# Optimization experiments

Hardware: AMD Instinct MI355X
Metric: run time of the kernel (lower is better)

The kernel has to match this reference:

```python
import jax, jax.numpy as jnp
import numpy as np

K = 8  # K_num: neighbors per pred point


def setup_inputs() -> dict:
    key = jax.random.key(0)
    ks = jax.random.split(key, 8)
    B, Nr, Np, C = 2, 8192, 8192, 256
    s = 1.0 / np.sqrt(C)
    return {
        "xyz_ref": jax.random.normal(ks[0], (B, Nr, 3), jnp.float32) * 10.0,
        "xyz_pred": jax.random.normal(ks[1], (B, Np, 3), jnp.float32) * 10.0,
        "feat_k_ref": jax.random.normal(ks[2], (B, Nr, C), jnp.float32),
        "feat_q_pred": jax.random.normal(ks[3], (B, Np, C), jnp.float32),
        "feat_v_ref": jax.random.normal(ks[4], (B, Nr, C), jnp.float32),
        "Wv": jax.random.normal(ks[5], (C, C), jnp.float32) * s,
        "bv": jnp.zeros((C,), jnp.float32),
        "Wo": jax.random.normal(ks[6], (C, C), jnp.float32) * s,
        "bo": jnp.zeros((C,), jnp.float32),
        "Wout": jax.random.normal(ks[7], (2 * C, C), jnp.float32) * s,
    }


def reference(xyz_ref, xyz_pred, feat_k_ref, feat_q_pred, feat_v_ref, Wv, bv, Wo, bo, Wout):
    B, Np, C = feat_q_pred.shape
    Nr = feat_k_ref.shape[1]

    # --- KNN search (torch.no_grad in original) ---
    xr = jax.lax.stop_gradient(xyz_ref)
    xp = jax.lax.stop_gradient(xyz_pred)
    d2 = (jnp.sum(xp * xp, -1)[:, :, None]
          + jnp.sum(xr * xr, -1)[:, None, :]
          - 2.0 * jnp.einsum('bpd,brd->bpr', xp, xr))  # [B, Np, Nr]
    _, idx = jax.lax.top_k(-d2, K)  # [B, Np, K] nearest ref indices per pred point

    # --- W_v (Conv1d 1x1) applied to all ref values before gather ---
    v_all = jnp.einsum('brc,dc->brd', feat_v_ref, Wv) + bv  # [B, Nr, C]

    gather = jax.vmap(lambda f, i: f[i])  # per-sample fancy gather
    k = gather(feat_k_ref, idx)  # [B, Np, K, C]
    v = gather(v_all, idx)       # [B, Np, K, C]

    # --- tiny per-point cross attention over K neighbors ---
    scores = jnp.einsum('bpc,bpkc->bpk', feat_q_pred, k) / jnp.sqrt(jnp.asarray(C, feat_q_pred.dtype))
    attn = jax.nn.softmax(scores, axis=-1)          # [B, Np, K]
    out = jnp.einsum('bpk,bpkc->bpc', attn, v)      # [B, Np, C]

    # --- W_o (Conv1d 1x1) ---
    out = jnp.einsum('bpc,dc->bpd', out, Wo) + bo   # [B, Np, C]

    # --- scatter into full point set: ref rows stay zero, pred rows get out ---
    out_all = jnp.concatenate([jnp.zeros((B, Nr, C), out.dtype), out], axis=1)  # [B, Nr+Np, C]

    # --- W_out (MinkowskiConvolution k=1, no bias): C -> 2C ---
    return jnp.einsum('bnc,dc->bnd', out_all, Wout)  # [B, Nr+Np, 2C]
```

## Files before the change

### kernel.cpp

```cpp
#include <hip/hip_runtime.h>
#include <stdint.h>


#define NRr 8192
#define NPp 8192
#define NC  256
#define NK  8
#define NCH   16
#define CHUNK 512

typedef short bf16x8 __attribute__((ext_vector_type(8)));
typedef float f32x4  __attribute__((ext_vector_type(4)));

__device__ __forceinline__ uint16_t f2bf(float f) {
  uint32_t u = __float_as_uint(f);
  return (uint16_t)((u + 0x7fffu + ((u >> 16) & 1u)) >> 16);
}

__device__ __forceinline__ float d2f(float px, float py, float pz, float sp, float4 r) {
  float m0 = __fmul_rn(px, r.x), m1 = __fmul_rn(py, r.y), m2 = __fmul_rn(pz, r.z);
  float dot = __fadd_rn(__fadd_rn(m0, m1), m2);
  return __fsub_rn(__fadd_rn(sp, r.w), __fadd_rn(dot, dot));
}

__device__ __forceinline__ float d2q(float px, float py, float pz, float sp, float4 r) {
  float dot = fmaf(px, r.x, fmaf(py, r.y, pz * r.z));
  return fmaf(-2.f, dot, sp + r.w);
}

#define SLACK 0.0625f

__device__ __forceinline__ uint32_t fkey(float f) {
  uint32_t b = __float_as_uint(f);
  return (b & 0x80000000u) ? ~b : (b | 0x80000000u);
}

__global__ __launch_bounds__(64) void k_prep(const float* __restrict__ xyz_ref,
                                             float4* __restrict__ ref4) {
  int i = blockIdx.x * 64 + threadIdx.x;
  if (i >= 2 * NRr) return;
  float x = xyz_ref[i*3+0];
  float y = xyz_ref[i*3+1];
  float z = xyz_ref[i*3+2];
  float n = __fadd_rn(__fadd_rn(__fmul_rn(x,x), __fmul_rn(y,y)), __fmul_rn(z,z));
  ref4[i] = make_float4(x, y, z, n);
}

__device__ __forceinline__ void insert8(float d2, int j, float (&dist)[8], int (&id)[8]) {
  if (d2 < dist[7]) {
    #pragma unroll
    for (int k = 7; k >= 1; --k) {
      bool sh = d2 < dist[k-1];
      bool pl = d2 < dist[k];
      float nd = sh ? dist[k-1] : (pl ? d2 : dist[k]);
      int   ni = sh ? id[k-1]   : (pl ? j  : id[k]);
      dist[k] = nd; id[k] = ni;
    }
    if (d2 < dist[0]) { dist[0] = d2; id[0] = j; }
  }
}

__global__ __launch_bounds__(256, 5) void k_knn(const float* __restrict__ xyz_pred,
                                                const float4* __restrict__ ref4,
                                                uint16_t* __restrict__ part,
                                                const float* __restrict__ Wv,
                                                const float* __restrict__ bv,
                                                const float* __restrict__ Wo,
                                                const float* __restrict__ bo,
                                                const float* __restrict__ Wout,
                                                uint16_t* __restrict__ Aw,
                                                float* __restrict__ bbig) {
  __shared__ __align__(16) char smem[32768];

  if (blockIdx.x < 64) {
    float (*M8)[256] = (float (*)[256])smem;
    float* red = (float*)(smem + 8192);
    int e0 = blockIdx.x * 8;
    int t  = threadIdx.x;

    float acc8[8];
    #pragma unroll
    for (int e = 0; e < 8; ++e) acc8[e] = 0.f;
    for (int d = 0; d < 256; ++d) {
      float wo = Wo[(size_t)d*256 + t];
      #pragma unroll
      for (int e = 0; e < 8; ++e)
        acc8[e] = fmaf(Wout[(size_t)(e0+e)*256 + d], wo, acc8[e]);
    }
    #pragma unroll
    for (int e = 0; e < 8; ++e) M8[e][t] = acc8[e];
    __syncthreads();

    float a8[8];
    #pragma unroll
    for (int e = 0; e < 8; ++e) a8[e] = 0.f;
    for (int c = 0; c < 256; ++c) {
      float wv = Wv[(size_t)c*256 + t];
      #pragma unroll
      for (int e = 0; e < 8; ++e)
        a8[e] = fmaf(M8[e][c], wv, a8[e]);
    }
    #pragma unroll
    for (int e = 0; e < 8; ++e) Aw[(size_t)(e0+e)*256 + t] = f2bf(a8[e]);

    for (int e = 0; e < 8; ++e) {
      red[t] = fmaf(M8[e][t], bv[t], Wout[(size_t)(e0+e)*256 + t] * bo[t]);
      __syncthreads();
      for (int s2 = 128; s2 > 0; s2 >>= 1) {
        if (t < s2) red[t] += red[t + s2];
        __syncthreads();
      }
      if (t == 0) bbig[e0+e] = red[0];
      __syncthreads();
    }
    return;
  }

  float4* sref = (float4*)smem;
  int wave = threadIdx.x >> 6;
  int lane = threadIdx.x & 63;
  int task = (blockIdx.x - 64) * 4 + wave;
  int ch   = task & (NCH - 1);
  int P    = (task >> 4) * 64 + lane;
  int b    = P >> 13;

  float px = xyz_pred[P*3+0];
  float py = xyz_pred[P*3+1];
  float pz = xyz_pred[P*3+2];
  float sp = __fadd_rn(__fadd_rn(__fmul_rn(px,px), __fmul_rn(py,py)), __fmul_rn(pz,pz));

  const float4* refbase = ref4 + (size_t)b * NRr;
  int rbase = ch * CHUNK;
  float4* srefw = sref + wave * CHUNK;
  for (int j = lane; j < CHUNK; j += 64) srefw[j] = refbase[rbase + j];

  float a0 = 3.4e38f, a1 = 3.4e38f, a2 = 3.4e38f, a3 = 3.4e38f;
  float g0 = 3.4e38f, g1 = 3.4e38f, g2 = 3.4e38f, g3 = 3.4e38f;
  float dist[8]; int id[8];
  #pragma unroll
  for (int k = 0; k < 8; ++k) { dist[k] = 3.4e38f; id[k] = 0; }

  for (int s = 0; s < CHUNK / 32; ++s) {
    uint32_t mm = 0;
    int base = s * 32;
    #pragma unroll 4
    for (int jj = 0; jj < 32; jj += 2) {
      float d0 = d2q(px, py, pz, sp, srefw[base + jj]);
      float d1 = d2q(px, py, pz, sp, srefw[base + jj + 1]);
      a3 = __builtin_amdgcn_fmed3f(d0, a2, a3);
      a2 = __builtin_amdgcn_fmed3f(d0, a1, a2);
      a1 = __builtin_amdgcn_fmed3f(d0, a0, a1);
      a0 = fminf(d0, a0);
      g3 = __builtin_amdgcn_fmed3f(d1, g2, g3);
      g2 = __builtin_amdgcn_fmed3f(d1, g1, g2);
      g1 = __builtin_amdgcn_fmed3f(d1, g0, g1);
      g0 = fminf(d1, g0);
      float tau = fmaxf(a3, g3) + SLACK;
      mm |= (uint32_t)(d0 <= tau) << jj;
      mm |= (uint32_t)(d1 <= tau) << (jj + 1);
    }
    while (mm) {
      int bit = __builtin_ctz(mm); mm &= mm - 1;
      int j = base + bit;
      float dd = d2f(px, py, pz, sp, srefw[j]);
      insert8(dd, j, dist, id);
    }
  }

  uint16_t* pp = part + ((size_t)P * NCH + ch) * 8;
  #pragma unroll
  for (int k = 0; k < 8; ++k)
    pp[k] = (uint16_t)((rbase + id[k]) & (NRr - 1));
}

__global__ __launch_bounds__(256) void k_attn(const float* __restrict__ feat_q,
    const float* __restrict__ feat_k, const float* __restrict__ feat_v,
    const uint16_t* __restrict__ part, const float* __restrict__ xyz_pred,
    const float4* __restrict__ ref4, uint16_t* __restrict__ g) {
  int wave = threadIdx.x >> 6;
  int lane = threadIdx.x & 63;
  int P = blockIdx.x * 4 + wave;
  int b = P >> 13;

  float px = xyz_pred[P*3+0];
  float py = xyz_pred[P*3+1];
  float pz = xyz_pred[P*3+2];
  float sp = __fadd_rn(__fadd_rn(__fmul_rn(px,px), __fmul_rn(py,py)), __fmul_rn(pz,pz));
  const float4* refbase = ref4 + (size_t)b * NRr;

  const uint32_t* pw = (const uint32_t*)(part + (size_t)P * (NCH * 8));
  uint32_t two = pw[lane];
  int j0 = two & (NRr - 1);
  int j1 = (two >> 16) & (NRr - 1);
  float d0 = d2f(px, py, pz, sp, refbase[j0]);
  float d1 = d2f(px, py, pz, sp, refbase[j1]);
  uint64_t k0 = ((uint64_t)fkey(d0) << 32) | (uint32_t)j0;
  uint64_t k1 = ((uint64_t)fkey(d1) << 32) | (uint32_t)j1;

  int nb[8];
  #pragma unroll
  for (int r = 0; r < 8; ++r) {
    uint64_t m = (k0 < k1) ? k0 : k1;
    #pragma unroll
    for (int s = 1; s < 64; s <<= 1) {
      uint64_t o = __shfl_xor(m, s, 64);
      m = (o < m) ? o : m;
    }
    nb[r] = (int)(uint32_t)(m & 0xFFFFFFFFu) & (NRr - 1);
    if (k0 == m) k0 = ~0ULL;
    if (k1 == m) k1 = ~0ULL;
  }

  float4 qv = *(const float4*)(feat_q + (size_t)P*NC + lane*4);
  const float* kb = feat_k + (size_t)b * NRr * NC;
  const float* vb = feat_v + (size_t)b * NRr * NC;

  float s[8];
  #pragma unroll
  for (int k = 0; k < 8; ++k) {
    float4 kv = *(const float4*)(kb + (size_t)nb[k]*NC + lane*4);
    float p = qv.x * kv.x;
    p = fmaf(qv.y, kv.y, p);
    p = fmaf(qv.z, kv.z, p);
    p = fmaf(qv.w, kv.w, p);
    s[k] = p;
  }
  #pragma unroll
  for (int k = 0; k < 8; ++k) {
    float v = s[k];
    #pragma unroll
    for (int m = 1; m < 64; m <<= 1) v += __shfl_xor(v, m, 64);
    s[k] = v * 0.0625f;
  }
  float mx = s[0];
  #pragma unroll
  for (int k = 1; k < 8; ++k) mx = fmaxf(mx, s[k]);
  float e[8], sum = 0.f;
  #pragma unroll
  for (int k = 0; k < 8; ++k) { e[k] = expf(s[k] - mx); sum += e[k]; }
  float inv = 1.0f / sum;

  float g0 = 0.f, g1 = 0.f, g2 = 0.f, g3 = 0.f;
  #pragma unroll
  for (int k = 0; k < 8; ++k) {
    float4 vv = *(const float4*)(vb + (size_t)nb[k]*NC + lane*4);
    float w = e[k] * inv;
    g0 = fmaf(w, vv.x, g0);
    g1 = fmaf(w, vv.y, g1);
    g2 = fmaf(w, vv.z, g2);
    g3 = fmaf(w, vv.w, g3);
  }
  uint32_t p0 = ((uint32_t)f2bf(g1) << 16) | f2bf(g0);
  uint32_t p1 = ((uint32_t)f2bf(g3) << 16) | f2bf(g2);
  *(uint2*)(g + (size_t)P*NC + lane*4) = make_uint2(p0, p1);
}

__global__ void k_zero(float4* __restrict__ o) {
  int i = blockIdx.x * 256 + threadIdx.x;
  int b = i >> 20;
  int r = i & 1048575;
  o[(size_t)b * 2097152 + r] = make_float4(0.f, 0.f, 0.f, 0.f);
}

__global__ __launch_bounds__(256) void k_gemm(const uint16_t* __restrict__ g,
    const uint16_t* __restrict__ Aw, const float* __restrict__ bbig,
    float* __restrict__ outp) {
  __shared__ __align__(16) uint16_t sA[64 * 136];
  __shared__ __align__(16) uint16_t sB[64 * 136];
  int t = threadIdx.x;
  int lane = t & 63, wave = t >> 6;
  int wm = (wave >> 1) * 32, wn = (wave & 1) * 32;
  int q = lane >> 4, rr = lane & 15;
  int bm = blockIdx.x;
  int bn = blockIdx.y;
  f32x4 zero = {0.f, 0.f, 0.f, 0.f};
  f32x4 acc[2][2] = {{zero, zero}, {zero, zero}};

  for (int ph = 0; ph < 2; ++ph) {
    #pragma unroll
    for (int i = 0; i < 4; ++i) {
      int cc  = t + i * 256;
      int row = cc >> 4;
      int col = (cc & 15) << 3;
      uint4 da = *(const uint4*)(g  + ((size_t)(bm*64 + row))*NC + ph*128 + col);
      *(uint4*)(&sA[row*136 + col]) = da;
      uint4 db = *(const uint4*)(Aw + ((size_t)(bn*64 + row))*NC + ph*128 + col);
      *(uint4*)(&sB[row*136 + col]) = db;
    }
    __syncthreads();
    #pragma unroll
    for (int kk = 0; kk < 4; ++kk) {
      int ko = kk*32 + q*8;
      bf16x8 a0 = *(const bf16x8*)(&sA[(wm      + rr)*136 + ko]);
      bf16x8 a1 = *(const bf16x8*)(&sA[(wm + 16 + rr)*136 + ko]);
      bf16x8 b0 = *(const bf16x8*)(&sB[(wn      + rr)*136 + ko]);
      bf16x8 b1 = *(const bf16x8*)(&sB[(wn + 16 + rr)*136 + ko]);
      acc[0][0] = __builtin_amdgcn_mfma_f32_16x16x32_bf16(a0, b0, acc[0][0], 0, 0, 0);
      acc[0][1] = __builtin_amdgcn_mfma_f32_16x16x32_bf16(a0, b1, acc[0][1], 0, 0, 0);
      acc[1][0] = __builtin_amdgcn_mfma_f32_16x16x32_bf16(a1, b0, acc[1][0], 0, 0, 0);
      acc[1][1] = __builtin_amdgcn_mfma_f32_16x16x32_bf16(a1, b1, acc[1][1], 0, 0, 0);
    }
    __syncthreads();
  }
  #pragma unroll
  for (int j = 0; j < 2; ++j) {
    int col = bn*64 + wn + j*16 + rr;
    float bias = bbig[col];
    #pragma unroll
    for (int i = 0; i < 2; ++i) {
      #pragma unroll
      for (int r = 0; r < 4; ++r) {
        int row = bm*64 + wm + i*16 + q*4 + r;
        float v = acc[i][j][r] + bias;
        int bb = row >> 13, p = row & 8191;
        outp[((size_t)(bb*16384 + 8192 + p))*512 + col] = v;
      }
    }
  }
}

extern "C" void kernel_launch(void* const* d_in, const int* in_sizes, int n_in,
                              void* d_out, int out_size, void* d_ws, size_t ws_size,
                              hipStream_t stream) {
  const float* xyz_ref  = (const float*)d_in[0];
  const float* xyz_pred = (const float*)d_in[1];
  const float* feat_k   = (const float*)d_in[2];
  const float* feat_q   = (const float*)d_in[3];
  const float* feat_v   = (const float*)d_in[4];
  const float* Wv       = (const float*)d_in[5];
  const float* bv       = (const float*)d_in[6];
  const float* Wo       = (const float*)d_in[7];
  const float* bo       = (const float*)d_in[8];
  const float* Wout     = (const float*)d_in[9];
  float* outp = (float*)d_out;

  char* ob = (char*)d_out;
  uint16_t* g    = (uint16_t*)ob;
  float4*   ref4 = (float4*)(ob + 8388608);
  uint16_t* Aw   = (uint16_t*)(ob + 9175040);
  float*    bbig = (float*)(ob + 9437184);
  uint16_t* part = (uint16_t*)(ob + 33554432);

  k_prep   <<<256,  64,  0, stream>>>(xyz_ref, ref4);
  k_knn    <<<1088, 256, 0, stream>>>(xyz_pred, ref4, part,
                                      Wv, bv, Wo, bo, Wout, Aw, bbig);
  k_attn   <<<4096, 256, 0, stream>>>(feat_q, feat_k, feat_v, part,
                                      xyz_pred, ref4, g);
  k_gemm   <<<dim3(256, 8), 256, 0, stream>>>(g, Aw, bbig, outp);
  k_zero   <<<8192, 256, 0, stream>>>((float4*)outp);
}
```

Baseline: 283.8 us.

## Assign one wave per pred point in KNN and merge top-8 inside the kernel

The KNN kernel used to give each lane its own pred point and split the ref set into 16 chunks, writing partial top-8 lists that k_attn then re-scored and merged. Now each wave handles a single pred point: lanes stride over shared-memory tiles of refs, each lane keeps a local top-8, and a wave-wide shuffle reduction produces the final 8 indices, which go straight to an idx buffer. k_attn reads only those indices, which removes the partial-list traffic and the recompute-and-merge step. The cost is more blocks with block-level syncs per tile and a per-point shuffle merge inside KNN.

```diff
diff --git a/kernel.cpp b/kernel.cpp
--- a/kernel.cpp
+++ b/kernel.cpp
@@ -6,8 +6,8 @@
 #define NPp 8192
 #define NC  256
 #define NK  8
-#define NCH   16
-#define CHUNK 512
+#define TILE 1024
+#define NT   8
 
 typedef short bf16x8 __attribute__((ext_vector_type(8)));
 typedef float f32x4  __attribute__((ext_vector_type(4)));
@@ -60,9 +60,9 @@
   }
 }
 
-__global__ __launch_bounds__(256, 5) void k_knn(const float* __restrict__ xyz_pred,
+__global__ __launch_bounds__(256, 8) void k_knn(const float* __restrict__ xyz_pred,
                                                 const float4* __restrict__ ref4,
-                                                uint16_t* __restrict__ part,
+                                                int* __restrict__ idx,
                                                 const float* __restrict__ Wv,
                                                 const float* __restrict__ bv,
                                                 const float* __restrict__ Wo,
@@ -70,7 +70,7 @@
                                                 const float* __restrict__ Wout,
                                                 uint16_t* __restrict__ Aw,
                                                 float* __restrict__ bbig) {
-  __shared__ __align__(16) char smem[32768];
+  __shared__ __align__(16) char smem[16384];
 
   if (blockIdx.x < 64) {
     float (*M8)[256] = (float (*)[256])smem;
@@ -116,12 +116,11 @@
     return;
   }
 
-  float4* sref = (float4*)smem;
+  float4* tile = (float4*)smem;
+  int kb   = blockIdx.x - 64;
   int wave = threadIdx.x >> 6;
   int lane = threadIdx.x & 63;
-  int task = (blockIdx.x - 64) * 4 + wave;
-  int ch   = task & (NCH - 1);
-  int P    = (task >> 4) * 64 + lane;
+  int P    = kb * 4 + wave;
   int b    = P >> 13;
 
   float px = xyz_pred[P*3+0];
@@ -130,9 +129,6 @@
   float sp = __fadd_rn(__fadd_rn(__fmul_rn(px,px), __fmul_rn(py,py)), __fmul_rn(pz,pz));
 
   const float4* refbase = ref4 + (size_t)b * NRr;
-  int rbase = ch * CHUNK;
-  float4* srefw = sref + wave * CHUNK;
-  for (int j = lane; j < CHUNK; j += 64) srefw[j] = refbase[rbase + j];
 
   float a0 = 3.4e38f, a1 = 3.4e38f, a2 = 3.4e38f, a3 = 3.4e38f;
   float g0 = 3.4e38f, g1 = 3.4e38f, g2 = 3.4e38f, g3 = 3.4e38f;
@@ -140,13 +136,20 @@
   #pragma unroll
   for (int k = 0; k < 8; ++k) { dist[k] = 3.4e38f; id[k] = 0; }
 
-  for (int s = 0; s < CHUNK / 32; ++s) {
+  for (int t = 0; t < NT; ++t) {
+    int tb = t * TILE;
+    #pragma unroll
+    for (int u = 0; u < 4; ++u)
+      tile[threadIdx.x + u*256] = refbase[tb + threadIdx.x + u*256];
+    __syncthreads();
+
     uint32_t mm = 0;
-    int base = s * 32;
     #pragma unroll 4
-    for (int jj = 0; jj < 32; jj += 2) {
-      float d0 = d2q(px, py, pz, sp, srefw[base + jj]);
-      float d1 = d2q(px, py, pz, sp, srefw[base + jj + 1]);
+    for (int i = 0; i < 16; i += 2) {
+      float4 r0 = tile[i*64 + lane];
+      float4 r1 = tile[(i+1)*64 + lane];
+      float d0 = d2q(px, py, pz, sp, r0);
+      float d1 = d2q(px, py, pz, sp, r1);
       a3 = __builtin_amdgcn_fmed3f(d0, a2, a3);
       a2 = __builtin_amdgcn_fmed3f(d0, a1, a2);
       a1 = __builtin_amdgcn_fmed3f(d0, a0, a1);
@@ -156,60 +159,52 @@
       g1 = __builtin_amdgcn_fmed3f(d1, g0, g1);
       g0 = fminf(d1, g0);
       float tau = fmaxf(a3, g3) + SLACK;
-      mm |= (uint32_t)(d0 <= tau) << jj;
-      mm |= (uint32_t)(d1 <= tau) << (jj + 1);
+      mm |= (uint32_t)(d0 <= tau) << i;
+      mm |= (uint32_t)(d1 <= tau) << (i + 1);
     }
     while (mm) {
-      int bit = __builtin_ctz(mm); mm &= mm - 1;
-      int j = base + bit;
-      float dd = d2f(px, py, pz, sp, srefw[j]);
+      int i = __builtin_ctz(mm); mm &= mm - 1;
+      int j = tb + i*64 + lane;
+      float dd = d2f(px, py, pz, sp, tile[i*64 + lane]);
       insert8(dd, j, dist, id);
     }
-  }
-
-  uint16_t* pp = part + ((size_t)P * NCH + ch) * 8;
-  #pragma unroll
-  for (int k = 0; k < 8; ++k)
-    pp[k] = (uint16_t)((rbase + id[k]) & (NRr - 1));
+    __syncthreads();
+  }
+
+  int my = 0;
+  #pragma unroll
+  for (int r = 0; r < 8; ++r) {
+    uint64_t key = ((uint64_t)fkey(dist[0]) << 32) | (uint32_t)id[0];
+    uint64_t m = key;
+    #pragma unroll
+    for (int s = 1; s < 64; s <<= 1) {
+      uint64_t o = __shfl_xor(m, s, 64);
+      m = (o < m) ? o : m;
+    }
+    if (lane == r) my = (int)(uint32_t)(m & 0xFFFFFFFFu);
+    bool win = (key == m);
+    #pragma unroll
+    for (int k = 0; k < 7; ++k) {
+      dist[k] = win ? dist[k+1] : dist[k];
+      id[k]   = win ? id[k+1]   : id[k];
+    }
+    dist[7] = win ? 3.4e38f : dist[7];
+    id[7]   = win ? 0       : id[7];
+  }
+  if (lane < 8) idx[(size_t)P*8 + lane] = my & (NRr - 1);
 }
 
 __global__ __launch_bounds__(256) void k_attn(const float* __restrict__ feat_q,
     const float* __restrict__ feat_k, const float* __restrict__ feat_v,
-    const uint16_t* __restrict__ part, const float* __restrict__ xyz_pred,
-    const float4* __restrict__ ref4, uint16_t* __restrict__ g) {
+    const int* __restrict__ idx, uint16_t* __restrict__ g) {
   int wave = threadIdx.x >> 6;
   int lane = threadIdx.x & 63;
   int P = blockIdx.x * 4 + wave;
   int b = P >> 13;
-
-  float px = xyz_pred[P*3+0];
-  float py = xyz_pred[P*3+1];
-  float pz = xyz_pred[P*3+2];
-  float sp = __fadd_rn(__fadd_rn(__fmul_rn(px,px), __fmul_rn(py,py)), __fmul_rn(pz,pz));
-  const float4* refbase = ref4 + (size_t)b * NRr;
-
-  const uint32_t* pw = (const uint32_t*)(part + (size_t)P * (NCH * 8));
-  uint32_t two = pw[lane];
-  int j0 = two & (NRr - 1);
-  int j1 = (two >> 16) & (NRr - 1);
-  float d0 = d2f(px, py, pz, sp, refbase[j0]);
-  float d1 = d2f(px, py, pz, sp, refbase[j1]);
-  uint64_t k0 = ((uint64_t)fkey(d0) << 32) | (uint32_t)j0;
-  uint64_t k1 = ((uint64_t)fkey(d1) << 32) | (uint32_t)j1;
-
+  const int* ip = idx + (size_t)P * 8;
   int nb[8];
   #pragma unroll
-  for (int r = 0; r < 8; ++r) {
-    uint64_t m = (k0 < k1) ? k0 : k1;
-    #pragma unroll
-    for (int s = 1; s < 64; s <<= 1) {
-      uint64_t o = __shfl_xor(m, s, 64);
-      m = (o < m) ? o : m;
-    }
-    nb[r] = (int)(uint32_t)(m & 0xFFFFFFFFu) & (NRr - 1);
-    if (k0 == m) k0 = ~0ULL;
-    if (k1 == m) k1 = ~0ULL;
-  }
+  for (int k = 0; k < 8; ++k) nb[k] = ip[k] & (NRr - 1);
 
   float4 qv = *(const float4*)(feat_q + (size_t)P*NC + lane*4);
   const float* kb = feat_k + (size_t)b * NRr * NC;
@@ -337,15 +332,14 @@
   char* ob = (char*)d_out;
   uint16_t* g    = (uint16_t*)ob;
   float4*   ref4 = (float4*)(ob + 8388608);
+  int*      idx  = (int*)(ob + 8650752);
   uint16_t* Aw   = (uint16_t*)(ob + 9175040);
   float*    bbig = (float*)(ob + 9437184);
-  uint16_t* part = (uint16_t*)(ob + 33554432);
 
   k_prep   <<<256,  64,  0, stream>>>(xyz_ref, ref4);
-  k_knn    <<<1088, 256, 0, stream>>>(xyz_pred, ref4, part,
+  k_knn    <<<4160, 256, 0, stream>>>(xyz_pred, ref4, idx,
                                       Wv, bv, Wo, bo, Wout, Aw, bbig);
-  k_attn   <<<4096, 256, 0, stream>>>(feat_q, feat_k, feat_v, part,
-                                      xyz_pred, ref4, g);
+  k_attn   <<<4096, 256, 0, stream>>>(feat_q, feat_k, feat_v, idx, g);
   k_gemm   <<<dim3(256, 8), 256, 0, stream>>>(g, Aw, bbig, outp);
   k_zero   <<<8192, 256, 0, stream>>>((float4*)outp);
 }
```

New measurement: 292.5 us. 1.03x slower.
